# Kernel optimization log

Hardware: AMD Instinct MI355X
Metric: run time of the kernel (lower is better)

## Reference

```python
import jax, jax.numpy as jnp
import numpy as np

N, E, HD, L, A = 50000, 600000, 128, 4, 50
EIN = 3 * HD + 1  # edge MLP input: [h_row, h_col, dist, lam_e]


def _p(k, shape, scale=0.05):
    return (scale * jax.random.normal(k, shape)).astype(jnp.float32)


def setup_inputs() -> dict:
    key = jax.random.key(0)
    ks = jax.random.split(key, 24)
    inp = {
        "z": jax.random.randint(ks[0], (N,), 0, A),
        "pos": jax.random.normal(ks[1], (N, 3), dtype=jnp.float32),
        "edge_index": jax.random.randint(ks[2], (2, E), 0, N),
        "lam": jax.random.uniform(ks[3], (), dtype=jnp.float32),
        "atom_embed": _p(ks[4], (A, HD), 1.0),
        "lam_w": _p(ks[5], (1, HD)),
        "lam_b": _p(ks[6], (HD,)),
        "edge_w1": _p(ks[7], (L, EIN, HD)),
        "edge_b1": jnp.zeros((L, HD), jnp.float32),
        "edge_w2": _p(ks[8], (L, HD, HD)),
        "edge_b2": jnp.zeros((L, HD), jnp.float32),
        "node_w1": _p(ks[9], (L, 2 * HD, HD)),
        "node_b1": jnp.zeros((L, HD), jnp.float32),
        "node_w2": _p(ks[10], (L, HD, HD)),
        "node_b2": jnp.zeros((L, HD), jnp.float32),
        "ln_g": jnp.ones((L, HD), jnp.float32),
        "ln_b": jnp.zeros((L, HD), jnp.float32),
        "head_w1": _p(ks[11], (HD, HD)),
        "head_b1": jnp.zeros((HD,), jnp.float32),
        "head_w2": _p(ks[12], (HD, 1)),
        "head_b2": jnp.zeros((1,), jnp.float32),
    }
    return inp


def _layernorm(x, g, b, eps=1e-5):
    mu = jnp.mean(x, -1, keepdims=True)
    var = jnp.mean(jnp.square(x - mu), -1, keepdims=True)
    return (x - mu) * jax.lax.rsqrt(var + eps) * g + b


def reference(z, pos, edge_index, lam, atom_embed, lam_w, lam_b,
              edge_w1, edge_b1, edge_w2, edge_b2,
              node_w1, node_b1, node_w2, node_b2, ln_g, ln_b,
              head_w1, head_b1, head_w2, head_b2):
    h = atom_embed[z]                                  # [N, HD]
    # lambda_embed(lam.expand(N,1)): same vector for every node
    lam_vec = lam * lam_w[0] + lam_b                    # [HD]
    lam_feat = jnp.broadcast_to(lam_vec, (h.shape[0], HD))
    h = h + lam_feat
    row, col = edge_index[0], edge_index[1]
    diff = pos[row] - pos[col]                          # [E, 3] (constant over layers)
    dist = jnp.sqrt(jnp.sum(diff * diff, -1, keepdims=True) + 1e-8)  # [E,1]
    lam_e = lam_feat[row]                               # [E, HD]
    for i in range(L):
        ein = jnp.concatenate([h[row], h[col], dist, lam_e], -1)      # [E, 3*HD+1]
        m = jax.nn.silu(ein @ edge_w1[i] + edge_b1[i])
        m = jax.nn.silu(m @ edge_w2[i] + edge_b2[i])                  # [E, HD]
        agg = jnp.zeros_like(h).at[row].add(m)                        # scatter-add
        u = jax.nn.silu(jnp.concatenate([h, agg], -1) @ node_w1[i] + node_b1[i])
        u = u @ node_w2[i] + node_b2[i]
        h = _layernorm(h + u, ln_g[i], ln_b[i])
    pooled = jnp.mean(h, 0, keepdims=True)              # [1, HD]
    out = jax.nn.silu(pooled @ head_w1 + head_b1) @ head_w2 + head_b2  # [1, 1]
    return out
```

## Files before the change

kernel.cpp:

```cpp
#include <hip/hip_runtime.h>
#include <cstdint>
#include <cstddef>

#define HD 128
#define NLAYER 4
#define EINDIM 385

typedef _Float16 f16x8 __attribute__((ext_vector_type(8)));
typedef _Float16 f16x4 __attribute__((ext_vector_type(4)));
typedef float f32x4 __attribute__((ext_vector_type(4)));

__device__ __forceinline__ float silu_f(float x) {
    float e = __expf(-x);
    return x * __builtin_amdgcn_rcpf(1.f + e);
}

__device__ __forceinline__ void lds_barrier() {
    asm volatile("s_waitcnt lgkmcnt(0)" ::: "memory");
    __builtin_amdgcn_s_barrier();
}

__global__ __launch_bounds__(128) void k_init(const float* __restrict__ lam_p,
                                              const float* __restrict__ lam_w,
                                              const float* __restrict__ lam_b,
                                              const float* __restrict__ edge_w1,
                                              const float* __restrict__ edge_b1,
                                              float* __restrict__ lam_vec,
                                              float* __restrict__ c1) {
    __shared__ float sl[HD];
    const int j = threadIdx.x;
    const int l = blockIdx.x;
    float lam = lam_p[0];
    float v = lam * lam_w[j] + lam_b[j];
    sl[j] = v;
    if (l == 0) lam_vec[j] = v;
    __syncthreads();
    float acc = edge_b1[l * HD + j];
    const float* w = edge_w1 + ((size_t)l * EINDIM + 257) * HD + j;
#pragma unroll 8
    for (int k = 0; k < HD; k++) acc = fmaf(sl[k], w[(size_t)k * HD], acc);
    c1[l * HD + j] = acc;
}

__global__ void k_prep(const float* __restrict__ ew1, const float* __restrict__ ew2,
                       const float* __restrict__ nw1, const float* __restrict__ nw2,
                       _Float16* __restrict__ W1te, _Float16* __restrict__ W2te,
                       _Float16* __restrict__ W1tn, _Float16* __restrict__ W2tn,
                       float* __restrict__ wd) {
    int t = blockIdx.x * 256 + threadIdx.x;
    if (t < NLAYER * 128 * 256) {
        int l = t >> 15, r = t & 32767, j = r >> 8, k = r & 255;
        W1te[t] = (_Float16)ew1[((size_t)l * EINDIM + k) * HD + j];
        return;
    }
    t -= NLAYER * 128 * 256;
    if (t < NLAYER * 128 * 256) {
        int l = t >> 15, r = t & 32767, j = r >> 8, k = r & 255;
        W1tn[t] = (_Float16)nw1[((size_t)l * 256 + k) * HD + j];
        return;
    }
    t -= NLAYER * 128 * 256;
    if (t < NLAYER * 128 * 128) {
        int l = t >> 14, r = t & 16383, j = r >> 7, k = r & 127;
        W2te[t] = (_Float16)ew2[((size_t)l * 128 + k) * HD + j];
        return;
    }
    t -= NLAYER * 128 * 128;
    if (t < NLAYER * 128 * 128) {
        int l = t >> 14, r = t & 16383, j = r >> 7, k = r & 127;
        W2tn[t] = (_Float16)nw2[((size_t)l * 128 + k) * HD + j];
        return;
    }
    t -= NLAYER * 128 * 128;
    if (t < NLAYER * 128) {
        int l = t >> 7, j = t & 127;
        wd[t] = ew1[((size_t)l * EINDIM + 256) * HD + j];
    }
}

__global__ void k_embed(const int* __restrict__ z,
                        const float* __restrict__ atom_embed,
                        const float* __restrict__ lam_vec,
                        float* __restrict__ h, _Float16* __restrict__ hh, int n4) {
    int i = blockIdx.x * 256 + threadIdx.x;
    if (i >= n4) return;
    int n = i >> 5, q = i & 31;
    int a = z[n];
    float4 e = *(const float4*)&atom_embed[(size_t)a * HD + q * 4];
    float4 lv = *(const float4*)&lam_vec[q * 4];
    e.x += lv.x; e.y += lv.y; e.z += lv.z; e.w += lv.w;
    *(float4*)&h[(size_t)n * HD + q * 4] = e;
    f16x4 hv;
    hv[0] = (_Float16)e.x; hv[1] = (_Float16)e.y;
    hv[2] = (_Float16)e.z; hv[3] = (_Float16)e.w;
    *(f16x4*)&hh[(size_t)n * HD + q * 4] = hv;
}

__global__ void k_zero(float4* __restrict__ p, int n4) {
    for (int i = blockIdx.x * 256 + threadIdx.x; i < n4; i += gridDim.x * 256)
        p[i] = make_float4(0.f, 0.f, 0.f, 0.f);
}

__global__ void k_hist(const int* __restrict__ ei, int* __restrict__ deg, int E) {
    int e = blockIdx.x * 256 + threadIdx.x;
    if (e < E) atomicAdd(&deg[ei[e]], 1);
}

__global__ __launch_bounds__(1024) void k_scan(const int* __restrict__ deg,
                                               int* __restrict__ cursor, int N) {
    __shared__ int part[1024];
    int t = threadIdx.x;
    int chunk = (N + 1023) >> 10;
    int s0 = t * chunk, s1 = s0 + chunk;
    if (s1 > N) s1 = N;
    int s = 0;
    for (int i = s0; i < s1; i++) s += deg[i];
    part[t] = s;
    __syncthreads();
    for (int d = 1; d < 1024; d <<= 1) {
        int v = (t >= d) ? part[t - d] : 0;
        __syncthreads();
        part[t] += v;
        __syncthreads();
    }
    int base = (t == 0) ? 0 : part[t - 1];
    for (int i = s0; i < s1; i++) {
        cursor[i] = base;
        base += deg[i];
    }
}

__global__ void k_scatter(const int* __restrict__ ei, int* __restrict__ cursor,
                          int* __restrict__ perm, int E) {
    int e = blockIdx.x * 256 + threadIdx.x;
    if (e < E) {
        int p = atomicAdd(&cursor[ei[e]], 1);
        perm[p] = e;
    }
}

__global__ void k_apply(const int* __restrict__ perm, const int* __restrict__ ei,
                        const float* __restrict__ pos,
                        int* __restrict__ rowS, int* __restrict__ colS,
                        float* __restrict__ distS, int E, int Epad) {
    int i = blockIdx.x * 256 + threadIdx.x;
    if (i >= Epad) return;
    if (i < E) {
        int e = perm[i];
        int r = ei[e], c = ei[E + e];
        rowS[i] = r; colS[i] = c;
        float dx = pos[r * 3 + 0] - pos[c * 3 + 0];
        float dy = pos[r * 3 + 1] - pos[c * 3 + 1];
        float dz = pos[r * 3 + 2] - pos[c * 3 + 2];
        distS[i] = sqrtf(dx * dx + dy * dy + dz * dz + 1e-8f);
    } else {
        rowS[i] = -1; colS[i] = 0; distS[i] = 0.f;
    }
}

__global__ void k_mask(const int* __restrict__ rowS,
                       unsigned long long* __restrict__ maskBuf, int Epad) {
    int i = blockIdx.x * 256 + threadIdx.x;
    if (i >= Epad) return;
    bool pred = (i + 1 >= Epad) ? true : (rowS[i] != rowS[i + 1]);
    unsigned long long m = __ballot(pred);
    if ((i & 63) == 0) maskBuf[i >> 6] = m;
}

__global__ __launch_bounds__(256, 2) void k_edge_mfma(
    const _Float16* __restrict__ hh,
    const int* __restrict__ rowS, const int* __restrict__ colS,
    const float* __restrict__ distS,
    const unsigned long long* __restrict__ maskBuf,
    int Epad, int ntiles, int tpb,
    const _Float16* __restrict__ W1t,
    const _Float16* __restrict__ W2t,
    const float* __restrict__ wd, const float* __restrict__ c1,
    const float* __restrict__ b2,
    float* __restrict__ agg) {
    __shared__ __align__(16) _Float16 shA[64 * 264];
    __shared__ __align__(16) _Float16 shM[64 * 136];
    __shared__ int shRow2[2][64];
    __shared__ float shD2[2][64];
    __shared__ float shWd[HD], shC1[HD], shB2[HD];

    const int tid = threadIdx.x;
    const int w = tid >> 6, l = tid & 63;
    const int lg = l >> 4, lr = l & 15;

    f16x8 w1f[2][8], w2f[2][4];
#pragma unroll
    for (int cf = 0; cf < 2; cf++) {
        const int col = w * 32 + cf * 16 + lr;
#pragma unroll
        for (int s = 0; s < 8; s++)
            w1f[cf][s] = *(const f16x8*)(W1t + (size_t)col * 256 + s * 32 + lg * 8);
#pragma unroll
        for (int s = 0; s < 4; s++)
            w2f[cf][s] = *(const f16x8*)(W2t + (size_t)col * 128 + s * 32 + lg * 8);
    }
    if (tid < 128) { shWd[tid] = wd[tid]; shC1[tid] = c1[tid]; }
    else shB2[tid - 128] = b2[tid - 128];

    const int t0 = blockIdx.x * tpb;
    int t1 = t0 + tpb; if (t1 > ntiles) t1 = ntiles;
    if (t0 >= t1) return;

    int idxv[8];
    f16x8 vA[8];
    int rv = -1; float dv = 0.f;

    {
        const int e0 = t0 * 64;
#pragma unroll
        for (int it = 0; it < 8; it++) {
            int flat = tid + it * 256;
            int e = flat >> 5, c = flat & 31;
            idxv[it] = (c < 16) ? rowS[e0 + e] : colS[e0 + e];
        }
        if (tid < 64) { rv = rowS[e0 + tid]; dv = distS[e0 + tid]; }
#pragma unroll
        for (int it = 0; it < 8; it++) {
            int idx = idxv[it]; if (idx < 0) idx = 0;
            int c = (tid + it * 256) & 31;
            int cc = (c < 16) ? c : (c - 16);
            vA[it] = *(const f16x8*)(hh + (size_t)idx * HD + cc * 8);
        }
        int tn = t0 + 1; if (tn > ntiles - 1) tn = ntiles - 1;
        const int e0n = tn * 64;
#pragma unroll
        for (int it = 0; it < 8; it++) {
            int flat = tid + it * 256;
            int e = flat >> 5, c = flat & 31;
            idxv[it] = (c < 16) ? rowS[e0n + e] : colS[e0n + e];
        }
    }
    __syncthreads();

    for (int t = t0; t < t1; t++) {
        const int pb = t & 1;
        const unsigned long long bmCur = maskBuf[t];
        const unsigned long long bmPrev = (t > 0) ? maskBuf[t - 1] : ~0ull;

#pragma unroll
        for (int it = 0; it < 8; it++) {
            int flat = tid + it * 256;
            int e = flat >> 5, c = flat & 31;
            *(f16x8*)&shA[e * 264 + c * 8] = vA[it];
        }
        if (tid < 64) { shRow2[pb][tid] = rv; shD2[pb][tid] = dv; }

        {
            int tn = t + 1; if (tn > ntiles - 1) tn = ntiles - 1;
            const int e0n = tn * 64;
#pragma unroll
            for (int it = 0; it < 8; it++) {
                int idx = idxv[it]; if (idx < 0) idx = 0;
                int c = (tid + it * 256) & 31;
                int cc = (c < 16) ? c : (c - 16);
                vA[it] = *(const f16x8*)(hh + (size_t)idx * HD + cc * 8);
            }
            if (tid < 64) { rv = rowS[e0n + tid]; dv = distS[e0n + tid]; }
            int tn2 = t + 2; if (tn2 > ntiles - 1) tn2 = ntiles - 1;
            const int e0n2 = tn2 * 64;
#pragma unroll
            for (int it = 0; it < 8; it++) {
                int flat = tid + it * 256;
                int e = flat >> 5, c = flat & 31;
                idxv[it] = (c < 16) ? rowS[e0n2 + e] : colS[e0n2 + e];
            }
        }

        lds_barrier();

        f32x4 acc[4][2];
#pragma unroll
        for (int rf = 0; rf < 4; rf++)
#pragma unroll
            for (int cf = 0; cf < 2; cf++) acc[rf][cf] = (f32x4){0.f, 0.f, 0.f, 0.f};

#pragma unroll
        for (int s = 0; s < 8; s++) {
#pragma unroll
            for (int rf = 0; rf < 4; rf++) {
                f16x8 a = *(const f16x8*)&shA[(rf * 16 + lr) * 264 + s * 32 + lg * 8];
                acc[rf][0] = __builtin_amdgcn_mfma_f32_16x16x32_f16(a, w1f[0][s], acc[rf][0], 0, 0, 0);
                acc[rf][1] = __builtin_amdgcn_mfma_f32_16x16x32_f16(a, w1f[1][s], acc[rf][1], 0, 0, 0);
            }
        }
#pragma unroll
        for (int rf = 0; rf < 4; rf++)
#pragma unroll
            for (int cf = 0; cf < 2; cf++) {
                const int col = w * 32 + cf * 16 + lr;
#pragma unroll
                for (int r = 0; r < 4; r++) {
                    int row = rf * 16 + lg * 4 + r;
                    float x = acc[rf][cf][r] + shD2[pb][row] * shWd[col] + shC1[col];
                    shM[row * 136 + col] = (_Float16)silu_f(x);
                }
            }
        lds_barrier();

        f32x4 acc2[4][2];
#pragma unroll
        for (int rf = 0; rf < 4; rf++)
#pragma unroll
            for (int cf = 0; cf < 2; cf++) acc2[rf][cf] = (f32x4){0.f, 0.f, 0.f, 0.f};

#pragma unroll
        for (int s = 0; s < 4; s++) {
#pragma unroll
            for (int rf = 0; rf < 4; rf++) {
                f16x8 a = *(const f16x8*)&shM[(rf * 16 + lr) * 136 + s * 32 + lg * 8];
                acc2[rf][0] = __builtin_amdgcn_mfma_f32_16x16x32_f16(a, w2f[0][s], acc2[rf][0], 0, 0, 0);
                acc2[rf][1] = __builtin_amdgcn_mfma_f32_16x16x32_f16(a, w2f[1][s], acc2[rf][1], 0, 0, 0);
            }
        }
        lds_barrier();

#pragma unroll
        for (int rf = 0; rf < 4; rf++)
#pragma unroll
            for (int cf = 0; cf < 2; cf++) {
                const int col = w * 32 + cf * 16 + lr;
#pragma unroll
                for (int r = 0; r < 4; r++) {
                    int row = rf * 16 + lg * 4 + r;
                    shM[row * 136 + col] = (_Float16)silu_f(acc2[rf][cf][r] + shB2[col]);
                }
            }
        lds_barrier();

        {
            const int col = tid & 127, half = tid >> 7;
            const int i0 = half << 5;
            const unsigned int mh = (unsigned int)(bmCur >> i0);
            bool open = half ? !((bmCur >> 31) & 1ull) : !((bmPrev >> 63) & 1ull);
            float s = 0.f;
#pragma unroll
            for (int ib = 0; ib < 8; ib++) {
                const int i = i0 + ib * 4;
                float v0 = (float)shM[(i + 0) * 136 + col];
                float v1 = (float)shM[(i + 1) * 136 + col];
                float v2 = (float)shM[(i + 2) * 136 + col];
                float v3 = (float)shM[(i + 3) * 136 + col];
#pragma unroll
                for (int q = 0; q < 4; q++) {
                    s += (q == 0) ? v0 : (q == 1) ? v1 : (q == 2) ? v2 : v3;
                    if (mh & (1u << (ib * 4 + q))) {
                        int rc = shRow2[pb][i + q];
                        if (rc >= 0) {
                            if (open) atomicAdd(&agg[(size_t)rc * HD + col], s);
                            else      agg[(size_t)rc * HD + col] = s;
                        }
                        s = 0.f;
                        open = false;
                    }
                }
            }
            if (!((mh >> 31) & 1u)) {
                int rc = shRow2[pb][i0 + 31];
                if (rc >= 0) atomicAdd(&agg[(size_t)rc * HD + col], s);
            }
        }
    }
}

__global__ __launch_bounds__(256, 3) void k_node_mfma(
    const _Float16* __restrict__ hh_in, float* __restrict__ agg, int N,
    int ntiles, int tpb,
    const _Float16* __restrict__ W1t,
    const _Float16* __restrict__ W2t,
    const float* __restrict__ b1, const float* __restrict__ b2,
    const float* __restrict__ lng, const float* __restrict__ lnb,
    float* __restrict__ h, _Float16* __restrict__ hh_out) {
    __shared__ __align__(16) _Float16 shA[64 * 264];
    __shared__ __align__(16) _Float16 shM[64 * 136];
    __shared__ float shB1[HD], shB2[HD], shG[HD], shBt[HD];

    const int tid = threadIdx.x;
    const int w = tid >> 6, l = tid & 63;
    const int lg = l >> 4, lr = l & 15;

    f16x8 w1f[2][8], w2f[2][4];
#pragma unroll
    for (int cf = 0; cf < 2; cf++) {
        const int col = w * 32 + cf * 16 + lr;
#pragma unroll
        for (int s = 0; s < 8; s++)
            w1f[cf][s] = *(const f16x8*)(W1t + (size_t)col * 256 + s * 32 + lg * 8);
#pragma unroll
        for (int s = 0; s < 4; s++)
            w2f[cf][s] = *(const f16x8*)(W2t + (size_t)col * 128 + s * 32 + lg * 8);
    }
    if (tid < 128) { shB1[tid] = b1[tid]; shB2[tid] = b2[tid]; }
    else { shG[tid - 128] = lng[tid - 128]; shBt[tid - 128] = lnb[tid - 128]; }
    __syncthreads();

    int t1 = blockIdx.x * tpb + tpb;
    if (t1 > ntiles) t1 = ntiles;
    for (int t = blockIdx.x * tpb; t < t1; t++) {
        const int n0 = t * 64;

#pragma unroll
        for (int it = 0; it < 8; it++) {
            int flat = tid + it * 256;
            int e = flat >> 5, c = flat & 31;
            int n = n0 + e;
            f16x8 v = {};
            if (n < N) {
                if (c < 16) {
                    v = *(const f16x8*)(hh_in + (size_t)n * HD + c * 8);
                } else {
                    float* s = agg + (size_t)n * HD + (c - 16) * 8;
                    float4 v0 = *(const float4*)s;
                    float4 v1 = *(const float4*)(s + 4);
                    v[0] = (_Float16)v0.x; v[1] = (_Float16)v0.y;
                    v[2] = (_Float16)v0.z; v[3] = (_Float16)v0.w;
                    v[4] = (_Float16)v1.x; v[5] = (_Float16)v1.y;
                    v[6] = (_Float16)v1.z; v[7] = (_Float16)v1.w;
                    float4 z4 = make_float4(0.f, 0.f, 0.f, 0.f);
                    *(float4*)s = z4;
                    *(float4*)(s + 4) = z4;
                }
            }
            *(f16x8*)&shA[e * 264 + c * 8] = v;
        }
        lds_barrier();

        f32x4 acc[4][2];
#pragma unroll
        for (int rf = 0; rf < 4; rf++)
#pragma unroll
            for (int cf = 0; cf < 2; cf++) acc[rf][cf] = (f32x4){0.f, 0.f, 0.f, 0.f};

#pragma unroll
        for (int s = 0; s < 8; s++) {
#pragma unroll
            for (int rf = 0; rf < 4; rf++) {
                f16x8 a = *(const f16x8*)&shA[(rf * 16 + lr) * 264 + s * 32 + lg * 8];
                acc[rf][0] = __builtin_amdgcn_mfma_f32_16x16x32_f16(a, w1f[0][s], acc[rf][0], 0, 0, 0);
                acc[rf][1] = __builtin_amdgcn_mfma_f32_16x16x32_f16(a, w1f[1][s], acc[rf][1], 0, 0, 0);
            }
        }
#pragma unroll
        for (int rf = 0; rf < 4; rf++)
#pragma unroll
            for (int cf = 0; cf < 2; cf++) {
                const int col = w * 32 + cf * 16 + lr;
#pragma unroll
                for (int r = 0; r < 4; r++) {
                    int row = rf * 16 + lg * 4 + r;
                    shM[row * 136 + col] = (_Float16)silu_f(acc[rf][cf][r] + shB1[col]);
                }
            }
        lds_barrier();

        f32x4 acc2[4][2];
#pragma unroll
        for (int rf = 0; rf < 4; rf++)
#pragma unroll
            for (int cf = 0; cf < 2; cf++) acc2[rf][cf] = (f32x4){0.f, 0.f, 0.f, 0.f};

#pragma unroll
        for (int s = 0; s < 4; s++) {
#pragma unroll
            for (int rf = 0; rf < 4; rf++) {
                f16x8 a = *(const f16x8*)&shM[(rf * 16 + lr) * 136 + s * 32 + lg * 8];
                acc2[rf][0] = __builtin_amdgcn_mfma_f32_16x16x32_f16(a, w2f[0][s], acc2[rf][0], 0, 0, 0);
                acc2[rf][1] = __builtin_amdgcn_mfma_f32_16x16x32_f16(a, w2f[1][s], acc2[rf][1], 0, 0, 0);
            }
        }
        lds_barrier();

#pragma unroll
        for (int rf = 0; rf < 4; rf++)
#pragma unroll
            for (int cf = 0; cf < 2; cf++) {
                const int col = w * 32 + cf * 16 + lr;
#pragma unroll
                for (int r = 0; r < 4; r++) {
                    int row = rf * 16 + lg * 4 + r;
                    shM[row * 136 + col] = (_Float16)(acc2[rf][cf][r] + shB2[col]);
                }
            }
        lds_barrier();

        {
            int row = tid >> 2, q = tid & 3, n = n0 + row;
            float s = 0.f, ss = 0.f;
            if (n < N) {
#pragma unroll
                for (int j = 0; j < 8; j++) {
                    float4 hv = *(const float4*)&h[(size_t)n * HD + q * 32 + j * 4];
                    int cb = q * 32 + j * 4;
                    f16x4 uv = *(const f16x4*)&shM[row * 136 + cb];
                    float x0 = (float)uv[0] + hv.x;
                    float x1 = (float)uv[1] + hv.y;
                    float x2 = (float)uv[2] + hv.z;
                    float x3 = (float)uv[3] + hv.w;
                    s += x0 + x1 + x2 + x3;
                    ss += x0 * x0 + x1 * x1 + x2 * x2 + x3 * x3;
                }
            }
            s += __shfl_xor(s, 1);  s += __shfl_xor(s, 2);
            ss += __shfl_xor(ss, 1); ss += __shfl_xor(ss, 2);
            float mean = s * (1.f / 128.f);
            float var = ss * (1.f / 128.f) - mean * mean;
            float rstd = rsqrtf(var + 1e-5f);
            if (n < N) {
#pragma unroll
                for (int j = 0; j < 8; j++) {
                    float4 hv = *(const float4*)&h[(size_t)n * HD + q * 32 + j * 4];
                    int cb = q * 32 + j * 4;
                    f16x4 uv = *(const f16x4*)&shM[row * 136 + cb];
                    float4 y;
                    y.x = ((float)uv[0] + hv.x - mean) * rstd * shG[cb + 0] + shBt[cb + 0];
                    y.y = ((float)uv[1] + hv.y - mean) * rstd * shG[cb + 1] + shBt[cb + 1];
                    y.z = ((float)uv[2] + hv.z - mean) * rstd * shG[cb + 2] + shBt[cb + 2];
                    y.w = ((float)uv[3] + hv.w - mean) * rstd * shG[cb + 3] + shBt[cb + 3];
                    *(float4*)&h[(size_t)n * HD + cb] = y;
                    f16x4 yh;
                    yh[0] = (_Float16)y.x; yh[1] = (_Float16)y.y;
                    yh[2] = (_Float16)y.z; yh[3] = (_Float16)y.w;
                    *(f16x4*)&hh_out[(size_t)n * HD + cb] = yh;
                }
            }
        }
    }
}

__global__ __launch_bounds__(256) void k_pool1(const float* __restrict__ h,
                                               float* __restrict__ partial,
                                               int N, int RPB) {
    int bk = blockIdx.x, t = threadIdx.x;
    int j = t & 127, half = t >> 7;
    float s = 0.f;
    int rend = (bk + 1) * RPB; if (rend > N) rend = N;
    for (int r = bk * RPB + half; r < rend; r += 2) s += h[(size_t)r * HD + j];
    __shared__ float sh[256];
    sh[t] = s;
    __syncthreads();
    if (t < 128) partial[bk * HD + j] = sh[t] + sh[t + 128];
}

__global__ __launch_bounds__(128) void k_head(const float* __restrict__ partial,
                                              int nPart, int N,
                                              const float* __restrict__ hw1,
                                              const float* __restrict__ hb1,
                                              const float* __restrict__ hw2,
                                              const float* __restrict__ hb2,
                                              float* __restrict__ out) {
    __shared__ float pooled[HD];
    __shared__ float t1[HD];
    int j = threadIdx.x;
    double s = 0.0;
    for (int bk = 0; bk < nPart; bk++) s += (double)partial[bk * HD + j];
    pooled[j] = (float)(s / (double)N);
    __syncthreads();
    float acc = hb1[j];
    for (int k = 0; k < HD; k++) acc = fmaf(pooled[k], hw1[k * HD + j], acc);
    t1[j] = silu_f(acc) * hw2[j];
    __syncthreads();
    if (j < 64) t1[j] += t1[j + 64];
    __syncthreads();
    if (j < 64) {
        float v = t1[j];
#pragma unroll
        for (int o = 32; o > 0; o >>= 1) v += __shfl_xor(v, o);
        if (j == 0) out[0] = v + hb2[0];
    }
}

extern "C" void kernel_launch(void* const* d_in, const int* in_sizes, int n_in,
                              void* d_out, int out_size, void* d_ws, size_t ws_size,
                              hipStream_t stream) {
    const int* z      = (const int*)d_in[0];
    const float* pos  = (const float*)d_in[1];
    const int* ei     = (const int*)d_in[2];
    const float* lam  = (const float*)d_in[3];
    const float* aemb = (const float*)d_in[4];
    const float* lamw = (const float*)d_in[5];
    const float* lamb = (const float*)d_in[6];
    const float* ew1  = (const float*)d_in[7];
    const float* eb1  = (const float*)d_in[8];
    const float* ew2  = (const float*)d_in[9];
    const float* eb2  = (const float*)d_in[10];
    const float* nw1  = (const float*)d_in[11];
    const float* nb1  = (const float*)d_in[12];
    const float* nw2  = (const float*)d_in[13];
    const float* nb2  = (const float*)d_in[14];
    const float* lng  = (const float*)d_in[15];
    const float* lnb  = (const float*)d_in[16];
    const float* hw1  = (const float*)d_in[17];
    const float* hb1  = (const float*)d_in[18];
    const float* hw2  = (const float*)d_in[19];
    const float* hb2  = (const float*)d_in[20];

    const int N = in_sizes[0];
    const int E = in_sizes[2] / 2;
    const int etiles = (E + 63) / 64;
    const int Epad = etiles * 64;
    const int ntilesN = (N + 63) / 64;

    char* ws = (char*)d_ws;
    size_t off = 0;
    auto alloc = [&](size_t bytes) { void* p = ws + off; off += (bytes + 255) & ~(size_t)255; return p; };
    float* h        = (float*)alloc((size_t)N * HD * 4);
    float* agg      = (float*)alloc((size_t)N * HD * 4);
    _Float16* hh    = (_Float16*)alloc((size_t)N * HD * 2);
    int* deg        = (int*)alloc((size_t)N * 4);
    int* cursor     = (int*)alloc((size_t)N * 4);
    int* perm       = (int*)alloc((size_t)E * 4);
    int* rowS       = (int*)alloc((size_t)Epad * 4);
    int* colS       = (int*)alloc((size_t)Epad * 4);
    float* distS    = (float*)alloc((size_t)Epad * 4);
    unsigned long long* maskBuf = (unsigned long long*)alloc((size_t)etiles * 8);
    float* lamv     = (float*)alloc(HD * 4);
    float* c1       = (float*)alloc(NLAYER * HD * 4);
    float* wd       = (float*)alloc(NLAYER * HD * 4);
    float* part     = (float*)alloc(256 * HD * 4);
    _Float16* W1te  = (_Float16*)alloc((size_t)NLAYER * 128 * 256 * 2);
    _Float16* W1tn  = (_Float16*)alloc((size_t)NLAYER * 128 * 256 * 2);
    _Float16* W2te  = (_Float16*)alloc((size_t)NLAYER * 128 * 128 * 2);
    _Float16* W2tn  = (_Float16*)alloc((size_t)NLAYER * 128 * 128 * 2);

    k_init<<<NLAYER, 128, 0, stream>>>(lam, lamw, lamb, ew1, eb1, lamv, c1);
    int prepTot = NLAYER * 128 * 256 * 2 + NLAYER * 128 * 128 * 2 + NLAYER * 128;
    k_prep<<<(prepTot + 255) / 256, 256, 0, stream>>>(ew1, ew2, nw1, nw2,
                                                      W1te, W2te, W1tn, W2tn, wd);
    int n4 = N * 32;
    k_embed<<<(n4 + 255) / 256, 256, 0, stream>>>(z, aemb, lamv, h, hh, n4);

    k_zero<<<64, 256, 0, stream>>>((float4*)deg, (N + 3) / 4);
    k_hist<<<(E + 255) / 256, 256, 0, stream>>>(ei, deg, E);
    k_scan<<<1, 1024, 0, stream>>>(deg, cursor, N);
    k_scatter<<<(E + 255) / 256, 256, 0, stream>>>(ei, cursor, perm, E);
    k_apply<<<(Epad + 255) / 256, 256, 0, stream>>>(perm, ei, pos, rowS, colS, distS, E, Epad);
    k_mask<<<(Epad + 255) / 256, 256, 0, stream>>>(rowS, maskBuf, Epad);

    int zero4 = N * (HD / 4);
    k_zero<<<2048, 256, 0, stream>>>((float4*)agg, zero4);

    const int egrid = (etiles < 512) ? etiles : 512;
    const int etpb = (etiles + egrid - 1) / egrid;
    const int ngrid = (ntilesN + 1) / 2;
    for (int l = 0; l < NLAYER; l++) {
        k_edge_mfma<<<egrid, 256, 0, stream>>>(hh, rowS, colS, distS, maskBuf,
            Epad, etiles, etpb,
            W1te + (size_t)l * 128 * 256, W2te + (size_t)l * 128 * 128,
            wd + l * HD, c1 + l * HD, eb2 + l * HD, agg);
        k_node_mfma<<<ngrid, 256, 0, stream>>>(hh, agg, N, ntilesN, 2,
            W1tn + (size_t)l * 128 * 256, W2tn + (size_t)l * 128 * 128,
            nb1 + l * HD, nb2 + l * HD, lng + l * HD, lnb + l * HD, h, hh);
    }
    int RPB = (N + 255) / 256;
    k_pool1<<<256, 256, 0, stream>>>(h, part, N, RPB);
    k_head<<<1, 128, 0, stream>>>(part, 256, N, hw1, hb1, hw2, hb2, (float*)d_out);
}
```

Baseline: 981.3 us.

## Use 512-thread edge blocks with one 16-column slice per wave

```diff
diff --git a/kernel.cpp b/kernel.cpp
--- a/kernel.cpp
+++ b/kernel.cpp
@@ -167,7 +167,7 @@
     if ((i & 63) == 0) maskBuf[i >> 6] = m;
 }
 
-__global__ __launch_bounds__(256, 2) void k_edge_mfma(
+__global__ __launch_bounds__(512, 4) void k_edge_mfma(
     const _Float16* __restrict__ hh,
     const int* __restrict__ rowS, const int* __restrict__ colS,
     const float* __restrict__ distS,
@@ -187,52 +187,36 @@
     const int tid = threadIdx.x;
     const int w = tid >> 6, l = tid & 63;
     const int lg = l >> 4, lr = l & 15;
-
-    f16x8 w1f[2][8], w2f[2][4];
-#pragma unroll
-    for (int cf = 0; cf < 2; cf++) {
-        const int col = w * 32 + cf * 16 + lr;
-#pragma unroll
-        for (int s = 0; s < 8; s++)
-            w1f[cf][s] = *(const f16x8*)(W1t + (size_t)col * 256 + s * 32 + lg * 8);
-#pragma unroll
-        for (int s = 0; s < 4; s++)
-            w2f[cf][s] = *(const f16x8*)(W2t + (size_t)col * 128 + s * 32 + lg * 8);
-    }
+    const int col = w * 16 + lr;
+
+    f16x8 w1f[8], w2f[4];
+#pragma unroll
+    for (int s = 0; s < 8; s++)
+        w1f[s] = *(const f16x8*)(W1t + (size_t)col * 256 + s * 32 + lg * 8);
+#pragma unroll
+    for (int s = 0; s < 4; s++)
+        w2f[s] = *(const f16x8*)(W2t + (size_t)col * 128 + s * 32 + lg * 8);
     if (tid < 128) { shWd[tid] = wd[tid]; shC1[tid] = c1[tid]; }
-    else shB2[tid - 128] = b2[tid - 128];
+    else if (tid < 256) shB2[tid - 128] = b2[tid - 128];
 
     const int t0 = blockIdx.x * tpb;
     int t1 = t0 + tpb; if (t1 > ntiles) t1 = ntiles;
     if (t0 >= t1) return;
 
-    int idxv[8];
-    f16x8 vA[8];
+    f16x8 vA[4];
     int rv = -1; float dv = 0.f;
 
     {
         const int e0 = t0 * 64;
-#pragma unroll
-        for (int it = 0; it < 8; it++) {
-            int flat = tid + it * 256;
+        if (tid < 64) { rv = rowS[e0 + tid]; dv = distS[e0 + tid]; }
+#pragma unroll
+        for (int it = 0; it < 4; it++) {
+            int flat = tid + it * 512;
             int e = flat >> 5, c = flat & 31;
-            idxv[it] = (c < 16) ? rowS[e0 + e] : colS[e0 + e];
-        }
-        if (tid < 64) { rv = rowS[e0 + tid]; dv = distS[e0 + tid]; }
-#pragma unroll
-        for (int it = 0; it < 8; it++) {
-            int idx = idxv[it]; if (idx < 0) idx = 0;
-            int c = (tid + it * 256) & 31;
+            int idx = (c < 16) ? rowS[e0 + e] : colS[e0 + e];
+            if (idx < 0) idx = 0;
             int cc = (c < 16) ? c : (c - 16);
             vA[it] = *(const f16x8*)(hh + (size_t)idx * HD + cc * 8);
-        }
-        int tn = t0 + 1; if (tn > ntiles - 1) tn = ntiles - 1;
-        const int e0n = tn * 64;
-#pragma unroll
-        for (int it = 0; it < 8; it++) {
-            int flat = tid + it * 256;
-            int e = flat >> 5, c = flat & 31;
-            idxv[it] = (c < 16) ? rowS[e0n + e] : colS[e0n + e];
         }
     }
     __syncthreads();
@@ -243,8 +227,8 @@
         const unsigned long long bmPrev = (t > 0) ? maskBuf[t - 1] : ~0ull;
 
 #pragma unroll
-        for (int it = 0; it < 8; it++) {
-            int flat = tid + it * 256;
+        for (int it = 0; it < 4; it++) {
+            int flat = tid + it * 512;
             int e = flat >> 5, c = flat & 31;
             *(f16x8*)&shA[e * 264 + c * 8] = vA[it];
         }
@@ -254,114 +238,94 @@
             int tn = t + 1; if (tn > ntiles - 1) tn = ntiles - 1;
             const int e0n = tn * 64;
 #pragma unroll
-            for (int it = 0; it < 8; it++) {
-                int idx = idxv[it]; if (idx < 0) idx = 0;
-                int c = (tid + it * 256) & 31;
+            for (int it = 0; it < 4; it++) {
+                int flat = tid + it * 512;
+                int e = flat >> 5, c = flat & 31;
+                int idx = (c < 16) ? rowS[e0n + e] : colS[e0n + e];
+                if (idx < 0) idx = 0;
                 int cc = (c < 16) ? c : (c - 16);
                 vA[it] = *(const f16x8*)(hh + (size_t)idx * HD + cc * 8);
             }
             if (tid < 64) { rv = rowS[e0n + tid]; dv = distS[e0n + tid]; }
-            int tn2 = t + 2; if (tn2 > ntiles - 1) tn2 = ntiles - 1;
-            const int e0n2 = tn2 * 64;
-#pragma unroll
-            for (int it = 0; it < 8; it++) {
-                int flat = tid + it * 256;
-                int e = flat >> 5, c = flat & 31;
-                idxv[it] = (c < 16) ? rowS[e0n2 + e] : colS[e0n2 + e];
-            }
-        }
-
-        lds_barrier();
-
-        f32x4 acc[4][2];
-#pragma unroll
-        for (int rf = 0; rf < 4; rf++)
-#pragma unroll
-            for (int cf = 0; cf < 2; cf++) acc[rf][cf] = (f32x4){0.f, 0.f, 0.f, 0.f};
+        }
+
+        lds_barrier();
+
+        f32x4 acc[4];
+#pragma unroll
+        for (int rf = 0; rf < 4; rf++) acc[rf] = (f32x4){0.f, 0.f, 0.f, 0.f};
 
 #pragma unroll
         for (int s = 0; s < 8; s++) {
 #pragma unroll
             for (int rf = 0; rf < 4; rf++) {
                 f16x8 a = *(const f16x8*)&shA[(rf * 16 + lr) * 264 + s * 32 + lg * 8];
-                acc[rf][0] = __builtin_amdgcn_mfma_f32_16x16x32_f16(a, w1f[0][s], acc[rf][0], 0, 0, 0);
-                acc[rf][1] = __builtin_amdgcn_mfma_f32_16x16x32_f16(a, w1f[1][s], acc[rf][1], 0, 0, 0);
-            }
-        }
-#pragma unroll
-        for (int rf = 0; rf < 4; rf++)
-#pragma unroll
-            for (int cf = 0; cf < 2; cf++) {
-                const int col = w * 32 + cf * 16 + lr;
-#pragma unroll
-                for (int r = 0; r < 4; r++) {
-                    int row = rf * 16 + lg * 4 + r;
-                    float x = acc[rf][cf][r] + shD2[pb][row] * shWd[col] + shC1[col];
-                    shM[row * 136 + col] = (_Float16)silu_f(x);
-                }
-            }
-        lds_barrier();
-
-        f32x4 acc2[4][2];
-#pragma unroll
-        for (int rf = 0; rf < 4; rf++)
-#pragma unroll
-            for (int cf = 0; cf < 2; cf++) acc2[rf][cf] = (f32x4){0.f, 0.f, 0.f, 0.f};
+                acc[rf] = __builtin_amdgcn_mfma_f32_16x16x32_f16(a, w1f[s], acc[rf], 0, 0, 0);
+            }
+        }
+#pragma unroll
+        for (int rf = 0; rf < 4; rf++) {
+#pragma unroll
+            for (int r = 0; r < 4; r++) {
+                int row = rf * 16 + lg * 4 + r;
+                float x = acc[rf][r] + shD2[pb][row] * shWd[col] + shC1[col];
+                shM[row * 136 + col] = (_Float16)silu_f(x);
+            }
+            acc[rf] = (f32x4){0.f, 0.f, 0.f, 0.f};
+        }
+        lds_barrier();
 
 #pragma unroll
         for (int s = 0; s < 4; s++) {
 #pragma unroll
             for (int rf = 0; rf < 4; rf++) {
                 f16x8 a = *(const f16x8*)&shM[(rf * 16 + lr) * 136 + s * 32 + lg * 8];
-                acc2[rf][0] = __builtin_amdgcn_mfma_f32_16x16x32_f16(a, w2f[0][s], acc2[rf][0], 0, 0, 0);
-                acc2[rf][1] = __builtin_amdgcn_mfma_f32_16x16x32_f16(a, w2f[1][s], acc2[rf][1], 0, 0, 0);
-            }
-        }
-        lds_barrier();
-
-#pragma unroll
-        for (int rf = 0; rf < 4; rf++)
-#pragma unroll
-            for (int cf = 0; cf < 2; cf++) {
-                const int col = w * 32 + cf * 16 + lr;
-#pragma unroll
-                for (int r = 0; r < 4; r++) {
-                    int row = rf * 16 + lg * 4 + r;
-                    shM[row * 136 + col] = (_Float16)silu_f(acc2[rf][cf][r] + shB2[col]);
-                }
-            }
+                acc[rf] = __builtin_amdgcn_mfma_f32_16x16x32_f16(a, w2f[s], acc[rf], 0, 0, 0);
+            }
+        }
+        lds_barrier();
+
+#pragma unroll
+        for (int rf = 0; rf < 4; rf++) {
+#pragma unroll
+            for (int r = 0; r < 4; r++) {
+                int row = rf * 16 + lg * 4 + r;
+                shM[row * 136 + col] = (_Float16)silu_f(acc[rf][r] + shB2[col]);
+            }
+        }
         lds_barrier();
 
         {
-            const int col = tid & 127, half = tid >> 7;
-            const int i0 = half << 5;
-            const unsigned int mh = (unsigned int)(bmCur >> i0);
-            bool open = half ? !((bmCur >> 31) & 1ull) : !((bmPrev >> 63) & 1ull);
+            const int scol = tid & 127, quarter = tid >> 7;
+            const int i0 = quarter << 4;
+            const unsigned int mh = (unsigned int)(bmCur >> i0) & 0xFFFFu;
+            bool open = (quarter == 0) ? !((bmPrev >> 63) & 1ull)
+                                       : !((bmCur >> (i0 - 1)) & 1ull);
             float s = 0.f;
 #pragma unroll
-            for (int ib = 0; ib < 8; ib++) {
+            for (int ib = 0; ib < 4; ib++) {
                 const int i = i0 + ib * 4;
-                float v0 = (float)shM[(i + 0) * 136 + col];
-                float v1 = (float)shM[(i + 1) * 136 + col];
-                float v2 = (float)shM[(i + 2) * 136 + col];
-                float v3 = (float)shM[(i + 3) * 136 + col];
+                float v0 = (float)shM[(i + 0) * 136 + scol];
+                float v1 = (float)shM[(i + 1) * 136 + scol];
+                float v2 = (float)shM[(i + 2) * 136 + scol];
+                float v3 = (float)shM[(i + 3) * 136 + scol];
 #pragma unroll
                 for (int q = 0; q < 4; q++) {
                     s += (q == 0) ? v0 : (q == 1) ? v1 : (q == 2) ? v2 : v3;
                     if (mh & (1u << (ib * 4 + q))) {
                         int rc = shRow2[pb][i + q];
                         if (rc >= 0) {
-                            if (open) atomicAdd(&agg[(size_t)rc * HD + col], s);
-                            else      agg[(size_t)rc * HD + col] = s;
+                            if (open) atomicAdd(&agg[(size_t)rc * HD + scol], s);
+                            else      agg[(size_t)rc * HD + scol] = s;
                         }
                         s = 0.f;
                         open = false;
                     }
                 }
             }
-            if (!((mh >> 31) & 1u)) {
-                int rc = shRow2[pb][i0 + 31];
-                if (rc >= 0) atomicAdd(&agg[(size_t)rc * HD + col], s);
+            if (!((mh >> 15) & 1u)) {
+                int rc = shRow2[pb][i0 + 15];
+                if (rc >= 0) atomicAdd(&agg[(size_t)rc * HD + scol], s);
             }
         }
     }
@@ -647,7 +611,7 @@
     const int etpb = (etiles + egrid - 1) / egrid;
     const int ngrid = (ntilesN + 1) / 2;
     for (int l = 0; l < NLAYER; l++) {
-        k_edge_mfma<<<egrid, 256, 0, stream>>>(hh, rowS, colS, distS, maskBuf,
+        k_edge_mfma<<<egrid, 512, 0, stream>>>(hh, rowS, colS, distS, maskBuf,
             Epad, etiles, etpb,
             W1te + (size_t)l * 128 * 256, W2te + (size_t)l * 128 * 128,
             wd + l * HD, c1 + l * HD, eb2 + l * HD, agg);
```

New measurement: 958.9 us. 2.3% less time.
